# Kernel optimization log

Measured on AMD Instinct MI355X. Metric: run time of the kernel, lower is better.

The kernel has to match this reference:

```python
import jax, jax.numpy as jnp
import numpy as np

EPS = 1e-5  # torch BatchNorm2d default


def _conv1x1(x, w):
    # x: [n, cin, h, w], w: [cout, cin] (1x1 conv == per-pixel matmul)
    return jnp.einsum('nchw,oc->nohw', x, w)


def _bn(x, gamma, beta, mean, var):
    # inference-mode BatchNorm2d over channel dim
    scale = gamma * jax.lax.rsqrt(var + EPS)
    shift = beta - mean * scale
    return x * scale[None, :, None, None] + shift[None, :, None, None]


def setup_inputs() -> dict:
    key = jax.random.key(0)
    ks = jax.random.split(key, 24)
    n, c, h, w = 16, 256, 64, 64
    width, planes = c // 2, c
    inp = {
        'x': jax.random.normal(ks[0], (n, c, h, w), jnp.float32),
        'w_theta': jax.random.normal(ks[1], (width, c), jnp.float32) * 0.05,
        'w_phi': jax.random.normal(ks[2], (width, c), jnp.float32) * 0.05,
        'w_g': jax.random.normal(ks[3], (width, c), jnp.float32) * 0.05,
        'w_zeta': jax.random.normal(ks[4], (planes, width), jnp.float32) * 0.05,
    }
    for i, (name, dim) in enumerate([('bn1', width), ('bn2', width), ('bn3', width), ('bn4', planes)]):
        k = 5 + 4 * i
        inp[f'{name}_gamma'] = jax.random.uniform(ks[k], (dim,), jnp.float32, 0.5, 1.5)
        inp[f'{name}_beta'] = jax.random.normal(ks[k + 1], (dim,), jnp.float32) * 0.1
        inp[f'{name}_mean'] = jax.random.normal(ks[k + 2], (dim,), jnp.float32) * 0.1
        inp[f'{name}_var'] = jax.random.uniform(ks[k + 3], (dim,), jnp.float32, 0.5, 1.5)
    return inp


def reference(x, w_theta, w_phi, w_g, w_zeta,
              bn1_gamma, bn1_beta, bn1_mean, bn1_var,
              bn2_gamma, bn2_beta, bn2_mean, bn2_var,
              bn3_gamma, bn3_beta, bn3_mean, bn3_var,
              bn4_gamma, bn4_beta, bn4_mean, bn4_var):
    n, c, h, w = x.shape
    theta = jax.nn.relu(_bn(_conv1x1(x, w_theta), bn1_gamma, bn1_beta, bn1_mean, bn1_var))
    phi = jax.nn.relu(_bn(_conv1x1(x, w_phi), bn2_gamma, bn2_beta, bn2_mean, bn2_var))
    g = jax.nn.relu(_bn(_conv1x1(x, w_g), bn3_gamma, bn3_beta, bn3_mean, bn3_var))

    width = theta.shape[1]
    hw = h * w
    theta = theta.reshape(n, width, hw)  # [n, C', S]
    phi = phi.reshape(n, width, hw)      # [n, C', S]
    g = g.reshape(n, width, hw)          # [n, C', S]

    # (theta^T @ phi) @ g^T == theta^T @ (phi @ g^T): no softmax, so associativity
    # lets us contract over pixels first -> O(S*C'^2) instead of O(S^2*C').
    kv = jnp.einsum('ncs,nds->ncd', phi, g)      # [n, C', C']
    out = jnp.einsum('ncs,ncd->nsd', theta, kv)  # [n, S, C']

    # faithful to torch: reshape (not transpose) [n, S, C'] -> [n, C', h, w]
    out = out.reshape(n, width, h, w)
    out = _bn(_conv1x1(out, w_zeta), bn4_gamma, bn4_beta, bn4_mean, bn4_var)
    return jax.nn.relu(out + x)
```

## Files before the change

### kernel.cpp

```cpp
#include <hip/hip_runtime.h>

#define BN_EPS 1e-5f

typedef unsigned short u16;
typedef __bf16 bf16x8 __attribute__((ext_vector_type(8)));
typedef float floatx4 __attribute__((ext_vector_type(4)));
typedef u16 u16x4 __attribute__((ext_vector_type(4)));
typedef u16 u16x8 __attribute__((ext_vector_type(8)));

__device__ __forceinline__ u16 f2bf(float f) {
    union { float f; unsigned int u; } v; v.f = f;
    unsigned int r = (v.u + 0x7fffu + ((v.u >> 16) & 1u)) >> 16;
    return (u16)r;
}

__device__ __forceinline__ void gld16(const void* gsrc, void* ldst) {
    __builtin_amdgcn_global_load_lds(
        (const __attribute__((address_space(1))) unsigned int*)gsrc,
        (__attribute__((address_space(3))) unsigned int*)ldst, 16, 0, 0);
}

__device__ __forceinline__ int addsw(int seg, int s) {
    return (seg + (s & 7) + ((s >> 3) & 7)) & 7;
}

__global__ __launch_bounds__(256) void prep_kernel(
    const float* __restrict__ wt, const float* __restrict__ wp,
    const float* __restrict__ wg, const float* __restrict__ wz,
    const float* __restrict__ g1, const float* __restrict__ b1,
    const float* __restrict__ m1, const float* __restrict__ v1,
    const float* __restrict__ g2, const float* __restrict__ b2,
    const float* __restrict__ m2, const float* __restrict__ v2,
    const float* __restrict__ g3, const float* __restrict__ b3,
    const float* __restrict__ m3, const float* __restrict__ v3,
    const float* __restrict__ g4, const float* __restrict__ b4,
    const float* __restrict__ m4, const float* __restrict__ v4,
    u16* __restrict__ W1bf, float* __restrict__ shift1,
    u16* __restrict__ Wzbf, float* __restrict__ shift4)
{
    int id = blockIdx.x * 256 + threadIdx.x;
    if (id < 384 * 256) {
        int r = id >> 8, c = id & 255;
        int grp = r >> 7, ch = r & 127;
        const float* wsrc = grp == 0 ? wt : (grp == 1 ? wp : wg);
        const float* gg = grp == 0 ? g1 : (grp == 1 ? g2 : g3);
        const float* bb = grp == 0 ? b1 : (grp == 1 ? b2 : b3);
        const float* mm = grp == 0 ? m1 : (grp == 1 ? m2 : m3);
        const float* vv = grp == 0 ? v1 : (grp == 1 ? v2 : v3);
        float scale = gg[ch] * rsqrtf(vv[ch] + BN_EPS);
        W1bf[id] = f2bf(wsrc[ch * 256 + c] * scale);
        if (c == 0) shift1[r] = bb[ch] - mm[ch] * scale;
    }
    if (id < 256 * 128) {
        int o = id >> 7;
        float scale = g4[o] * rsqrtf(v4[o] + BN_EPS);
        Wzbf[id] = f2bf(wz[id] * scale);
        if ((id & 127) == 0) shift4[o] = b4[o] - m4[o] * scale;
    }
}

__global__ __launch_bounds__(256) void gemm1_kernel(
    const float* __restrict__ x, const u16* __restrict__ W1,
    const float* __restrict__ shift1,
    u16* __restrict__ theta_sm, u16* __restrict__ pg)
{
    const int st = blockIdx.x, mt = blockIdx.y, n = blockIdx.z;
    const int tid = threadIdx.x;
    const int w = tid >> 6, lane = tid & 63;
    const int quad = lane >> 4, l16 = lane & 15;

    __shared__ __align__(16) u16 ldsA[128 * 64];
    __shared__ __align__(16) u16 ldsB[128 * 64];

    floatx4 acc[2][8];
#pragma unroll
    for (int i = 0; i < 2; ++i)
#pragma unroll
        for (int j = 0; j < 8; ++j) acc[i][j] = floatx4{0.f, 0.f, 0.f, 0.f};

    const int s4 = tid & 31;
    const int cg = tid >> 5;
    const float* xbase = x + ((size_t)n * 256) * 4096 + st * 128;
    unsigned int* ldsBdw = (unsigned int*)ldsB;

    float4 xv0[4], xv1[4];
#pragma unroll
    for (int p = 0; p < 4; ++p) {
        int c0 = 2 * cg + 16 * p;
        xv0[p] = *((const float4*)(xbase + (size_t)c0 * 4096) + s4);
        xv1[p] = *((const float4*)(xbase + (size_t)(c0 + 1) * 4096) + s4);
    }

    for (int kc = 0; kc < 4; ++kc) {
#pragma unroll
        for (int p = 0; p < 4; ++p) {
            int cp = cg + 8 * p, slog = cp >> 2, dwin = cp & 3;
#pragma unroll
            for (int j = 0; j < 4; ++j) {
                int s = 4 * s4 + j;
                unsigned int pk = (unsigned int)f2bf(((const float*)&xv0[p])[j])
                                | ((unsigned int)f2bf(((const float*)&xv1[p])[j]) << 16);
                ldsBdw[s * 32 + addsw(slog, s) * 4 + dwin] = pk;
            }
        }
#pragma unroll
        for (int i = 0; i < 4; ++i) {
            int op = w * 4 + i;
            int r = op * 8 + (lane >> 3);
            int lseg = (lane & 7) ^ (r & 7);
            gld16(W1 + (size_t)(mt * 128 + r) * 256 + kc * 64 + lseg * 8,
                  ldsA + op * 512);
        }
        if (kc < 3) {
#pragma unroll
            for (int p = 0; p < 4; ++p) {
                int c0 = 2 * cg + 16 * p;
                xv0[p] = *((const float4*)(xbase + (size_t)((kc + 1) * 64 + c0) * 4096) + s4);
                xv1[p] = *((const float4*)(xbase + (size_t)((kc + 1) * 64 + c0 + 1) * 4096) + s4);
            }
        }
        __syncthreads();

#pragma unroll
        for (int kk = 0; kk < 2; ++kk) {
            bf16x8 a[2];
#pragma unroll
            for (int mi = 0; mi < 2; ++mi) {
                int r = w * 32 + mi * 16 + l16;
                int phys = (kk * 4 + quad) ^ (r & 7);
                a[mi] = *(const bf16x8*)(ldsA + r * 64 + phys * 8);
            }
#pragma unroll
            for (int ni = 0; ni < 8; ++ni) {
                int s = ni * 16 + l16;
                int phys = addsw(kk * 4 + quad, s);
                bf16x8 b = *(const bf16x8*)(ldsB + s * 64 + phys * 8);
#pragma unroll
                for (int mi = 0; mi < 2; ++mi)
                    acc[mi][ni] = __builtin_amdgcn_mfma_f32_16x16x32_bf16(
                        a[mi], b, acc[mi][ni], 0, 0, 0);
            }
        }
        __syncthreads();
    }

    if (mt == 0) {
#pragma unroll
        for (int mi = 0; mi < 2; ++mi) {
            int ocb = w * 32 + mi * 16 + quad * 4;
            float sh0 = shift1[ocb + 0], sh1 = shift1[ocb + 1];
            float sh2 = shift1[ocb + 2], sh3 = shift1[ocb + 3];
#pragma unroll
            for (int ni = 0; ni < 8; ++ni) {
                int s = st * 128 + ni * 16 + l16;
                float v0 = acc[mi][ni][0] + sh0, v1 = acc[mi][ni][1] + sh1;
                float v2 = acc[mi][ni][2] + sh2, v3 = acc[mi][ni][3] + sh3;
                u16x4 pk;
                pk[0] = f2bf(v0 > 0.f ? v0 : 0.f);
                pk[1] = f2bf(v1 > 0.f ? v1 : 0.f);
                pk[2] = f2bf(v2 > 0.f ? v2 : 0.f);
                pk[3] = f2bf(v3 > 0.f ? v3 : 0.f);
                *(u16x4*)(theta_sm + (size_t)n * 524288 + (size_t)s * 128 + ocb) = pk;
            }
        }
    } else {
#pragma unroll
        for (int mi = 0; mi < 2; ++mi)
#pragma unroll
            for (int r = 0; r < 4; ++r) {
                int oc = mt * 128 + w * 32 + mi * 16 + quad * 4 + r;
                int prow = (mt - 1) * 128 + w * 32 + mi * 16 + quad * 4 + r;
                float sh = shift1[oc];
#pragma unroll
                for (int ni = 0; ni < 8; ++ni) {
                    int s = st * 128 + ni * 16 + l16;
                    float val = acc[mi][ni][r] + sh;
                    val = val > 0.f ? val : 0.f;
                    pg[(size_t)n * 1048576 + (size_t)prow * 4096 + s] = f2bf(val);
                }
            }
    }
}

__global__ __launch_bounds__(512) void gemm2_kernel(
    const u16* __restrict__ pg, float* __restrict__ partials)
{
    const int kc = blockIdx.x, n = blockIdx.y;
    const int tid = threadIdx.x;
    const int w = tid >> 6, lane = tid & 63;
    const int quad = lane >> 4, l16 = lane & 15;

    __shared__ __align__(16) u16 ldsG[128 * 64];
    __shared__ __align__(16) u16 ldsP[128 * 64];

    floatx4 acc[2][4];
#pragma unroll
    for (int i = 0; i < 2; ++i)
#pragma unroll
        for (int j = 0; j < 4; ++j) acc[i][j] = floatx4{0.f, 0.f, 0.f, 0.f};

    const int d0 = (w >> 1) * 32, c0 = (w & 1) * 64;
    const u16* base = pg + (size_t)n * 1048576;

    for (int ch = 0; ch < 4; ++ch) {
        int s0 = kc * 256 + ch * 64;
#pragma unroll
        for (int i = 0; i < 2; ++i) {
            int op = w * 2 + i;
            int r = op * 8 + (lane >> 3);
            int lseg = (lane & 7) ^ (r & 7);
            gld16(base + (size_t)(128 + r) * 4096 + s0 + lseg * 8, ldsG + op * 512);
            gld16(base + (size_t)r * 4096 + s0 + lseg * 8, ldsP + op * 512);
        }
        __syncthreads();

#pragma unroll
        for (int kk = 0; kk < 2; ++kk) {
            bf16x8 a[2];
#pragma unroll
            for (int mi = 0; mi < 2; ++mi) {
                int r = d0 + mi * 16 + l16;
                int phys = (kk * 4 + quad) ^ (r & 7);
                a[mi] = *(const bf16x8*)(ldsG + r * 64 + phys * 8);
            }
#pragma unroll
            for (int ci = 0; ci < 4; ++ci) {
                int r = c0 + ci * 16 + l16;
                int phys = (kk * 4 + quad) ^ (r & 7);
                bf16x8 b = *(const bf16x8*)(ldsP + r * 64 + phys * 8);
#pragma unroll
                for (int mi = 0; mi < 2; ++mi)
                    acc[mi][ci] = __builtin_amdgcn_mfma_f32_16x16x32_bf16(
                        a[mi], b, acc[mi][ci], 0, 0, 0);
            }
        }
        __syncthreads();
    }

    float* outp = partials + (size_t)(n * 16 + kc) * 16384;
#pragma unroll
    for (int mi = 0; mi < 2; ++mi)
#pragma unroll
        for (int r = 0; r < 4; ++r) {
            int d = d0 + mi * 16 + quad * 4 + r;
#pragma unroll
            for (int ci = 0; ci < 4; ++ci)
                outp[d * 128 + c0 + ci * 16 + l16] = acc[mi][ci][r];
        }
}

__global__ __launch_bounds__(256) void kv_reduce_kernel(
    const float* __restrict__ partials, u16* __restrict__ kvT)
{
    int n = blockIdx.y;
    int f4 = blockIdx.x * 256 + threadIdx.x;
    const float4* p4 = (const float4*)partials;
    float4 s = {0.f, 0.f, 0.f, 0.f};
#pragma unroll
    for (int kc = 0; kc < 16; ++kc) {
        float4 v = p4[(size_t)(n * 16 + kc) * 4096 + f4];
        s.x += v.x; s.y += v.y; s.z += v.z; s.w += v.w;
    }
    u16x4 o; o[0] = f2bf(s.x); o[1] = f2bf(s.y); o[2] = f2bf(s.z); o[3] = f2bf(s.w);
    *(u16x4*)(kvT + (size_t)n * 16384 + f4 * 4) = o;
}

__global__ __launch_bounds__(256) void gemm3_kernel(
    const u16* __restrict__ theta_sm, const u16* __restrict__ kvT,
    u16* __restrict__ out_sd)
{
    const int st = blockIdx.x, n = blockIdx.y;
    const int tid = threadIdx.x;
    const int w = tid >> 6, lane = tid & 63;
    const int quad = lane >> 4, l16 = lane & 15;

    __shared__ __align__(16) u16 ldsT[128 * 64];
    __shared__ __align__(16) u16 ldsK[128 * 64];

    floatx4 acc[2][8];
#pragma unroll
    for (int i = 0; i < 2; ++i)
#pragma unroll
        for (int j = 0; j < 8; ++j) acc[i][j] = floatx4{0.f, 0.f, 0.f, 0.f};

    const u16* tbase = theta_sm + (size_t)n * 524288 + (size_t)st * 128 * 128;
    const u16* kbase = kvT + (size_t)n * 16384;

    for (int ch = 0; ch < 2; ++ch) {
#pragma unroll
        for (int i = 0; i < 4; ++i) {
            int op = w * 4 + i;
            int r = op * 8 + (lane >> 3);
            int lseg = (lane & 7) ^ (r & 7);
            gld16(tbase + (size_t)r * 128 + ch * 64 + lseg * 8, ldsT + op * 512);
            gld16(kbase + (size_t)r * 128 + ch * 64 + lseg * 8, ldsK + op * 512);
        }
        __syncthreads();

#pragma unroll
        for (int kk = 0; kk < 2; ++kk) {
            bf16x8 a[2];
#pragma unroll
            for (int mi = 0; mi < 2; ++mi) {
                int r = w * 32 + mi * 16 + l16;
                int phys = (kk * 4 + quad) ^ (r & 7);
                a[mi] = *(const bf16x8*)(ldsT + r * 64 + phys * 8);
            }
#pragma unroll
            for (int di = 0; di < 8; ++di) {
                int r = di * 16 + l16;
                int phys = (kk * 4 + quad) ^ (r & 7);
                bf16x8 b = *(const bf16x8*)(ldsK + r * 64 + phys * 8);
#pragma unroll
                for (int mi = 0; mi < 2; ++mi)
                    acc[mi][di] = __builtin_amdgcn_mfma_f32_16x16x32_bf16(
                        a[mi], b, acc[mi][di], 0, 0, 0);
            }
        }
        __syncthreads();
    }

#pragma unroll
    for (int mi = 0; mi < 2; ++mi)
#pragma unroll
        for (int r = 0; r < 4; ++r) {
            int s = st * 128 + w * 32 + mi * 16 + quad * 4 + r;
#pragma unroll
            for (int di = 0; di < 8; ++di)
                out_sd[(size_t)n * 524288 + (size_t)s * 128 + di * 16 + l16] =
                    f2bf(acc[mi][di][r]);
        }
}

__global__ __launch_bounds__(256) void gemm4_kernel(
    const u16* __restrict__ out_sd, const u16* __restrict__ Wz,
    const float* __restrict__ shift4, const float* __restrict__ x,
    float* __restrict__ out)
{
    const int st = blockIdx.x, ot = blockIdx.y, n = blockIdx.z;
    const int tid = threadIdx.x;
    const int w = tid >> 6, lane = tid & 63;
    const int quad = lane >> 4, l16 = lane & 15;

    __shared__ __align__(16) u16 ldsY[128 * 64];
    __shared__ __align__(16) u16 ldsW[128 * 64];

    floatx4 acc[2][8];
#pragma unroll
    for (int i = 0; i < 2; ++i)
#pragma unroll
        for (int j = 0; j < 8; ++j) acc[i][j] = floatx4{0.f, 0.f, 0.f, 0.f};

    const int sl = tid & 15;
    const int cg = tid >> 4;
    const u16* ybase = out_sd + (size_t)n * 524288 + st * 128;
    unsigned int* ldsYdw = (unsigned int*)ldsY;

    u16x8 yv0[2], yv1[2];
#pragma unroll
    for (int p = 0; p < 2; ++p) {
        int c0 = 2 * cg + 32 * p;
        yv0[p] = *(const u16x8*)(ybase + (size_t)c0 * 4096 + 8 * sl);
        yv1[p] = *(const u16x8*)(ybase + (size_t)(c0 + 1) * 4096 + 8 * sl);
    }

    for (int kc = 0; kc < 2; ++kc) {
#pragma unroll
        for (int p = 0; p < 2; ++p) {
            int cp = cg + 16 * p, slog = cp >> 2, dwin = cp & 3;
#pragma unroll
            for (int j = 0; j < 8; ++j) {
                int s = 8 * sl + j;
                unsigned int pk = (unsigned int)yv0[p][j] | ((unsigned int)yv1[p][j] << 16);
                ldsYdw[s * 32 + addsw(slog, s) * 4 + dwin] = pk;
            }
        }
#pragma unroll
        for (int i = 0; i < 4; ++i) {
            int op = w * 4 + i;
            int r = op * 8 + (lane >> 3);
            int lseg = (lane & 7) ^ (r & 7);
            gld16(Wz + (size_t)(ot * 128 + r) * 128 + kc * 64 + lseg * 8, ldsW + op * 512);
        }
        if (kc < 1) {
#pragma unroll
            for (int p = 0; p < 2; ++p) {
                int c0 = 2 * cg + 32 * p;
                yv0[p] = *(const u16x8*)(ybase + (size_t)(64 + c0) * 4096 + 8 * sl);
                yv1[p] = *(const u16x8*)(ybase + (size_t)(64 + c0 + 1) * 4096 + 8 * sl);
            }
        }
        __syncthreads();

#pragma unroll
        for (int kk = 0; kk < 2; ++kk) {
            bf16x8 a[2];
#pragma unroll
            for (int mi = 0; mi < 2; ++mi) {
                int r = w * 32 + mi * 16 + l16;
                int phys = (kk * 4 + quad) ^ (r & 7);
                a[mi] = *(const bf16x8*)(ldsW + r * 64 + phys * 8);
            }
#pragma unroll
            for (int ni = 0; ni < 8; ++ni) {
                int s = ni * 16 + l16;
                int phys = addsw(kk * 4 + quad, s);
                bf16x8 b = *(const bf16x8*)(ldsY + s * 64 + phys * 8);
#pragma unroll
                for (int mi = 0; mi < 2; ++mi)
                    acc[mi][ni] = __builtin_amdgcn_mfma_f32_16x16x32_bf16(
                        a[mi], b, acc[mi][ni], 0, 0, 0);
            }
        }
        __syncthreads();
    }

#pragma unroll
    for (int mi = 0; mi < 2; ++mi)
#pragma unroll
        for (int r = 0; r < 4; ++r) {
            int o = ot * 128 + w * 32 + mi * 16 + quad * 4 + r;
            float sh = shift4[o];
#pragma unroll
            for (int ni = 0; ni < 8; ++ni) {
                int s2 = st * 128 + ni * 16 + l16;
                size_t idx = ((size_t)n * 256 + o) * 4096 + s2;
                float val = acc[mi][ni][r] + sh + x[idx];
                out[idx] = val > 0.f ? val : 0.f;
            }
        }
}

extern "C" void kernel_launch(void* const* d_in, const int* in_sizes, int n_in,
                              void* d_out, int out_size, void* d_ws, size_t ws_size,
                              hipStream_t stream)
{
    const float* x  = (const float*)d_in[0];
    const float* wt = (const float*)d_in[1];
    const float* wp = (const float*)d_in[2];
    const float* wg = (const float*)d_in[3];
    const float* wz = (const float*)d_in[4];
    const float* bn[16];
    for (int i = 0; i < 16; ++i) bn[i] = (const float*)d_in[5 + i];

    char* ws = (char*)d_ws;
    u16*   W1bf     = (u16*)  (ws + 0);
    float* shift1   = (float*)(ws + 196608);
    u16*   Wzbf     = (u16*)  (ws + 198144);
    float* shift4   = (float*)(ws + 263680);
    u16*   theta_sm = (u16*)  (ws + 264704);
    u16*   pg       = (u16*)  (ws + 17041920);
    float* partials = (float*)(ws + 50596352);
    u16*   kvT      = (u16*)  (ws + 67373568);
    u16*   out_sd   = (u16*)  (ws + 67897856);
    float* out = (float*)d_out;

    prep_kernel<<<384, 256, 0, stream>>>(
        wt, wp, wg, wz,
        bn[0], bn[1], bn[2], bn[3],
        bn[4], bn[5], bn[6], bn[7],
        bn[8], bn[9], bn[10], bn[11],
        bn[12], bn[13], bn[14], bn[15],
        W1bf, shift1, Wzbf, shift4);

    gemm1_kernel<<<dim3(32, 3, 16), 256, 0, stream>>>(x, W1bf, shift1, theta_sm, pg);
    gemm2_kernel<<<dim3(16, 16), 512, 0, stream>>>(pg, partials);
    kv_reduce_kernel<<<dim3(16, 16), 256, 0, stream>>>(partials, kvT);
    gemm3_kernel<<<dim3(32, 16), 256, 0, stream>>>(theta_sm, kvT, out_sd);
    gemm4_kernel<<<dim3(32, 2, 16), 256, 0, stream>>>(out_sd, Wzbf, shift4, x, out);
}
```

Measured before the change: 218.2 us.

## Compute all three projections per block in gemm1 to avoid re-reading x

The first GEMM kernel now has each 512-thread block compute all 384 output channels (theta, phi, g) for a 64-pixel tile, instead of launching three M-tiles that each reload and convert the same x tile. This removes the threefold global read and fp32-to-bf16 conversion of x, with smaller pixel tiles and a larger weight tile in LDS. It also swaps the software bf16 rounding for the hardware v_cvt_pk_bf16_f32 instruction when packing. In exchange it uses more LDS per block and fewer total blocks, which may reduce occupancy.

```diff
diff --git a/kernel.cpp b/kernel.cpp
--- a/kernel.cpp
+++ b/kernel.cpp
@@ -12,6 +12,12 @@
     union { float f; unsigned int u; } v; v.f = f;
     unsigned int r = (v.u + 0x7fffu + ((v.u >> 16) & 1u)) >> 16;
     return (u16)r;
+}
+
+__device__ __forceinline__ unsigned int cvtpk(float lo, float hi) {
+    unsigned int r;
+    asm("v_cvt_pk_bf16_f32 %0, %1, %2" : "=v"(r) : "v"(lo), "v"(hi));
+    return r;
 }
 
 __device__ __forceinline__ void gld16(const void* gsrc, void* ldst) {
@@ -59,127 +65,114 @@
     }
 }
 
-__global__ __launch_bounds__(256) void gemm1_kernel(
+__global__ __launch_bounds__(512, 4) void gemm1_kernel(
     const float* __restrict__ x, const u16* __restrict__ W1,
     const float* __restrict__ shift1,
     u16* __restrict__ theta_sm, u16* __restrict__ pg)
 {
-    const int st = blockIdx.x, mt = blockIdx.y, n = blockIdx.z;
+    const int st = blockIdx.x, n = blockIdx.y;
     const int tid = threadIdx.x;
     const int w = tid >> 6, lane = tid & 63;
     const int quad = lane >> 4, l16 = lane & 15;
 
-    __shared__ __align__(16) u16 ldsA[128 * 64];
-    __shared__ __align__(16) u16 ldsB[128 * 64];
-
-    floatx4 acc[2][8];
-#pragma unroll
-    for (int i = 0; i < 2; ++i)
-#pragma unroll
-        for (int j = 0; j < 8; ++j) acc[i][j] = floatx4{0.f, 0.f, 0.f, 0.f};
-
-    const int s4 = tid & 31;
-    const int cg = tid >> 5;
-    const float* xbase = x + ((size_t)n * 256) * 4096 + st * 128;
+    __shared__ __align__(16) u16 ldsA[384 * 64];
+    __shared__ __align__(16) u16 ldsB[64 * 64];
+
+    floatx4 acc[3][4];
+#pragma unroll
+    for (int i = 0; i < 3; ++i)
+#pragma unroll
+        for (int j = 0; j < 4; ++j) acc[i][j] = floatx4{0.f, 0.f, 0.f, 0.f};
+
+    const int s4 = tid & 15;
+    const int cg = tid >> 4;
+    const int slog = cg >> 2, dwin = cg & 3;
+    const float* xb0 = x + ((size_t)n * 256 + 2 * cg) * 4096 + st * 64;
     unsigned int* ldsBdw = (unsigned int*)ldsB;
 
-    float4 xv0[4], xv1[4];
-#pragma unroll
-    for (int p = 0; p < 4; ++p) {
-        int c0 = 2 * cg + 16 * p;
-        xv0[p] = *((const float4*)(xbase + (size_t)c0 * 4096) + s4);
-        xv1[p] = *((const float4*)(xbase + (size_t)(c0 + 1) * 4096) + s4);
-    }
+    float4 xv0 = *((const float4*)xb0 + s4);
+    float4 xv1 = *((const float4*)(xb0 + 4096) + s4);
 
     for (int kc = 0; kc < 4; ++kc) {
-#pragma unroll
-        for (int p = 0; p < 4; ++p) {
-            int cp = cg + 8 * p, slog = cp >> 2, dwin = cp & 3;
-#pragma unroll
-            for (int j = 0; j < 4; ++j) {
-                int s = 4 * s4 + j;
-                unsigned int pk = (unsigned int)f2bf(((const float*)&xv0[p])[j])
-                                | ((unsigned int)f2bf(((const float*)&xv1[p])[j]) << 16);
-                ldsBdw[s * 32 + addsw(slog, s) * 4 + dwin] = pk;
-            }
-        }
-#pragma unroll
-        for (int i = 0; i < 4; ++i) {
-            int op = w * 4 + i;
+        const float* f0 = (const float*)&xv0;
+        const float* f1 = (const float*)&xv1;
+#pragma unroll
+        for (int j = 0; j < 4; ++j) {
+            int s = 4 * s4 + j;
+            ldsBdw[s * 32 + addsw(slog, s) * 4 + dwin] = cvtpk(f0[j], f1[j]);
+        }
+#pragma unroll
+        for (int i = 0; i < 6; ++i) {
+            int op = w * 6 + i;
             int r = op * 8 + (lane >> 3);
             int lseg = (lane & 7) ^ (r & 7);
-            gld16(W1 + (size_t)(mt * 128 + r) * 256 + kc * 64 + lseg * 8,
-                  ldsA + op * 512);
+            gld16(W1 + (size_t)r * 256 + kc * 64 + lseg * 8, ldsA + op * 512);
         }
         if (kc < 3) {
-#pragma unroll
-            for (int p = 0; p < 4; ++p) {
-                int c0 = 2 * cg + 16 * p;
-                xv0[p] = *((const float4*)(xbase + (size_t)((kc + 1) * 64 + c0) * 4096) + s4);
-                xv1[p] = *((const float4*)(xbase + (size_t)((kc + 1) * 64 + c0 + 1) * 4096) + s4);
-            }
+            xv0 = *((const float4*)(xb0 + (size_t)(kc + 1) * 64 * 4096) + s4);
+            xv1 = *((const float4*)(xb0 + (size_t)((kc + 1) * 64 + 1) * 4096) + s4);
         }
         __syncthreads();
 
 #pragma unroll
         for (int kk = 0; kk < 2; ++kk) {
-            bf16x8 a[2];
-#pragma unroll
-            for (int mi = 0; mi < 2; ++mi) {
-                int r = w * 32 + mi * 16 + l16;
-                int phys = (kk * 4 + quad) ^ (r & 7);
-                a[mi] = *(const bf16x8*)(ldsA + r * 64 + phys * 8);
-            }
-#pragma unroll
-            for (int ni = 0; ni < 8; ++ni) {
+            bf16x8 a[3];
+#pragma unroll
+            for (int mt = 0; mt < 3; ++mt) {
+                int r = mt * 128 + w * 16 + l16;
+                int phys = (kk * 4 + quad) ^ (r & 7);
+                a[mt] = *(const bf16x8*)(ldsA + r * 64 + phys * 8);
+            }
+#pragma unroll
+            for (int ni = 0; ni < 4; ++ni) {
                 int s = ni * 16 + l16;
                 int phys = addsw(kk * 4 + quad, s);
                 bf16x8 b = *(const bf16x8*)(ldsB + s * 64 + phys * 8);
 #pragma unroll
-                for (int mi = 0; mi < 2; ++mi)
-                    acc[mi][ni] = __builtin_amdgcn_mfma_f32_16x16x32_bf16(
-                        a[mi], b, acc[mi][ni], 0, 0, 0);
-            }
-        }
-        __syncthreads();
-    }
-
-    if (mt == 0) {
-#pragma unroll
-        for (int mi = 0; mi < 2; ++mi) {
-            int ocb = w * 32 + mi * 16 + quad * 4;
-            float sh0 = shift1[ocb + 0], sh1 = shift1[ocb + 1];
-            float sh2 = shift1[ocb + 2], sh3 = shift1[ocb + 3];
-#pragma unroll
-            for (int ni = 0; ni < 8; ++ni) {
-                int s = st * 128 + ni * 16 + l16;
-                float v0 = acc[mi][ni][0] + sh0, v1 = acc[mi][ni][1] + sh1;
-                float v2 = acc[mi][ni][2] + sh2, v3 = acc[mi][ni][3] + sh3;
-                u16x4 pk;
-                pk[0] = f2bf(v0 > 0.f ? v0 : 0.f);
-                pk[1] = f2bf(v1 > 0.f ? v1 : 0.f);
-                pk[2] = f2bf(v2 > 0.f ? v2 : 0.f);
-                pk[3] = f2bf(v3 > 0.f ? v3 : 0.f);
-                *(u16x4*)(theta_sm + (size_t)n * 524288 + (size_t)s * 128 + ocb) = pk;
-            }
-        }
-    } else {
-#pragma unroll
-        for (int mi = 0; mi < 2; ++mi)
-#pragma unroll
-            for (int r = 0; r < 4; ++r) {
-                int oc = mt * 128 + w * 32 + mi * 16 + quad * 4 + r;
-                int prow = (mt - 1) * 128 + w * 32 + mi * 16 + quad * 4 + r;
-                float sh = shift1[oc];
-#pragma unroll
-                for (int ni = 0; ni < 8; ++ni) {
-                    int s = st * 128 + ni * 16 + l16;
-                    float val = acc[mi][ni][r] + sh;
-                    val = val > 0.f ? val : 0.f;
-                    pg[(size_t)n * 1048576 + (size_t)prow * 4096 + s] = f2bf(val);
-                }
-            }
-    }
+                for (int mt = 0; mt < 3; ++mt)
+                    acc[mt][ni] = __builtin_amdgcn_mfma_f32_16x16x32_bf16(
+                        a[mt], b, acc[mt][ni], 0, 0, 0);
+            }
+        }
+        __syncthreads();
+    }
+
+    const int ocq = w * 16 + quad * 4;
+
+    {
+        float sh0 = shift1[ocq + 0], sh1 = shift1[ocq + 1];
+        float sh2 = shift1[ocq + 2], sh3 = shift1[ocq + 3];
+#pragma unroll
+        for (int ni = 0; ni < 4; ++ni) {
+            int s = st * 64 + ni * 16 + l16;
+            float v0 = acc[0][ni][0] + sh0, v1 = acc[0][ni][1] + sh1;
+            float v2 = acc[0][ni][2] + sh2, v3 = acc[0][ni][3] + sh3;
+            v0 = v0 > 0.f ? v0 : 0.f;
+            v1 = v1 > 0.f ? v1 : 0.f;
+            v2 = v2 > 0.f ? v2 : 0.f;
+            v3 = v3 > 0.f ? v3 : 0.f;
+            uint2 pk;
+            pk.x = cvtpk(v0, v1);
+            pk.y = cvtpk(v2, v3);
+            *(uint2*)(theta_sm + (size_t)n * 524288 + (size_t)s * 128 + ocq) = pk;
+        }
+    }
+
+#pragma unroll
+    for (int mt = 1; mt < 3; ++mt)
+#pragma unroll
+        for (int r = 0; r < 4; ++r) {
+            int oc = mt * 128 + ocq + r;
+            int prow = oc - 128;
+            float sh = shift1[oc];
+#pragma unroll
+            for (int ni = 0; ni < 4; ++ni) {
+                int s = st * 64 + ni * 16 + l16;
+                float val = acc[mt][ni][r] + sh;
+                val = val > 0.f ? val : 0.f;
+                pg[(size_t)n * 1048576 + (size_t)prow * 4096 + s] = f2bf(val);
+            }
+        }
 }
 
 __global__ __launch_bounds__(512) void gemm2_kernel(
@@ -463,7 +456,7 @@
         bn[12], bn[13], bn[14], bn[15],
         W1bf, shift1, Wzbf, shift4);
 
-    gemm1_kernel<<<dim3(32, 3, 16), 256, 0, stream>>>(x, W1bf, shift1, theta_sm, pg);
+    gemm1_kernel<<<dim3(64, 16), 512, 0, stream>>>(x, W1bf, shift1, theta_sm, pg);
     gemm2_kernel<<<dim3(16, 16), 512, 0, stream>>>(pg, partials);
     kv_reduce_kernel<<<dim3(16, 16), 256, 0, stream>>>(partials, kvT);
     gemm3_kernel<<<dim3(32, 16), 256, 0, stream>>>(theta_sm, kvT, out_sd);
```

Result: no change. 220.2 us (+0.9%).
